# Optimization experiments

Hardware: AMD Instinct MI355X
Metric: run time of the kernel (lower is better)

The kernel has to match this reference:

```python
import jax, jax.numpy as jnp
import numpy as np
from jax import lax

BN_EPS = 1e-5

def _conv(x, w, groups=1, pad=0):
    return lax.conv_general_dilated(
        x, w, window_strides=(1, 1), padding=[(pad, pad), (pad, pad)],
        dimension_numbers=('NCHW', 'OIHW', 'NCHW'), feature_group_count=groups)

def _gather2d(imgf, yi, xi, H, W):
    # imgf: [B,C,H*W] flattened image; yi, xi: [B,C,H,W] int32 corner indices
    valid = (yi >= 0) & (yi < H) & (xi >= 0) & (xi < W)
    yc = jnp.clip(yi, 0, H - 1)
    xc = jnp.clip(xi, 0, W - 1)
    idx = (yc * W + xc).reshape(imgf.shape[0], imgf.shape[1], -1)
    v = jnp.take_along_axis(imgf, idx, axis=2).reshape(yi.shape)
    return jnp.where(valid, v, 0.0)

def _bilinear_sample(img, y, x):
    # img: [B,C,H,W]; y, x: [B,C,H,W] float sample coords (zero outside)
    B, C, H, W = img.shape
    imgf = img.reshape(B, C, H * W)
    y0 = jnp.floor(y)
    x0 = jnp.floor(x)
    wy = y - y0  # weight for y1 corner
    wx = x - x0
    y0i = y0.astype(jnp.int32); y1i = y0i + 1
    x0i = x0.astype(jnp.int32); x1i = x0i + 1
    v00 = _gather2d(imgf, y0i, x0i, H, W)
    v01 = _gather2d(imgf, y0i, x1i, H, W)
    v10 = _gather2d(imgf, y1i, x0i, H, W)
    v11 = _gather2d(imgf, y1i, x1i, H, W)
    return ((1 - wy) * (1 - wx) * v00 + (1 - wy) * wx * v01
            + wy * (1 - wx) * v10 + wy * wx * v11)

def setup_inputs() -> dict:
    key = jax.random.key(0)
    ks = jax.random.split(key, 6)
    B, C, OC, H, W = 4, 64, 64, 256, 256
    return {
        'x': jax.random.normal(ks[0], (B, C, H, W), jnp.float32),
        'dw_weight': jax.random.normal(ks[1], (C, 1, 3, 3), jnp.float32) * 0.2,
        'pw_weight': jax.random.normal(ks[2], (3 * C, C, 1, 1), jnp.float32) * 0.1,
        'weight': jax.random.normal(ks[3], (OC, C, 1, 1), jnp.float32) * 0.1,
        'bias': jax.random.normal(ks[4], (OC,), jnp.float32) * 0.1,
        'gamma': jnp.ones((OC,), jnp.float32),
        'beta': jnp.zeros((OC,), jnp.float32),
    }

def reference(x, dw_weight, pw_weight, weight, bias, gamma, beta):
    B, C, H, W = x.shape
    # DWConv2d: depthwise 3x3 (pad 1) then pointwise 1x1 -> 3C channels
    om = _conv(_conv(x, dw_weight, groups=C, pad=1), pw_weight)
    offset_y = om[:, :C]
    offset_x = om[:, C:2 * C]
    modulator = 2.0 * jax.nn.sigmoid(om[:, 2 * C:])
    max_off = max(H, W) // 4
    offset = jnp.clip(jnp.concatenate([offset_y, offset_x], axis=1), -max_off, max_off)
    # torchvision deform_conv2d layout: [B, og*2, H, W] interleaved (y, x) per offset group
    off = offset.reshape(B, C, 2, H, W)
    hh = jnp.arange(H, dtype=x.dtype)[:, None]
    ww = jnp.arange(W, dtype=x.dtype)[None, :]
    sy = hh + off[:, :, 0]  # [B,C,H,W]
    sx = ww + off[:, :, 1]
    sampled = _bilinear_sample(x, sy, sx) * modulator
    w2 = weight.reshape(weight.shape[0], C)  # 1x1 kernel -> [OC, C]
    out = jnp.einsum('oc,bchw->bohw', w2, sampled) + bias[None, :, None, None]
    # BatchNorm2d (training-mode batch stats) + exact GELU
    mean = out.mean(axis=(0, 2, 3), keepdims=True)
    var = out.var(axis=(0, 2, 3), keepdims=True)
    out = (out - mean) * lax.rsqrt(var + BN_EPS)
    out = out * gamma[None, :, None, None] + beta[None, :, None, None]
    return jax.nn.gelu(out, approximate=False)
```

## Files before the change

kernel.cpp:

```cpp
#include <hip/hip_runtime.h>

#define B_  4
#define C_  64
#define H_  256
#define W_  256
#define HW_ 65536
#define NPIX_ (B_*HW_)
#define NELEM_ (B_*C_*HW_)

#define OMS 200
#define TS  72

typedef __attribute__((ext_vector_type(8))) short short8;
typedef __attribute__((ext_vector_type(4))) float floatx4;

static __device__ __forceinline__ unsigned short f2bf(float f){
  unsigned u = __float_as_uint(f);
  u += 0x7fff + ((u >> 16) & 1);
  return (unsigned short)(u >> 16);
}
static __device__ __forceinline__ float bf2f(unsigned short s){
  return __uint_as_float(((unsigned)s) << 16);
}
static __device__ __forceinline__ unsigned pack2(float a, float b){
  return (unsigned)f2bf(a) | ((unsigned)f2bf(b) << 16);
}

__global__ __launch_bounds__(256) void k_cvtw(
    const float* __restrict__ pw, const float* __restrict__ w2,
    unsigned short* __restrict__ wB)
{
  int i = blockIdx.x*256 + threadIdx.x;
  wB[i] = f2bf(i < 12288 ? pw[i] : w2[i - 12288]);
}

__global__ __launch_bounds__(256) void k_cvtx(
    const float4* __restrict__ X4, uint2* __restrict__ Y)
{
  int i = blockIdx.x*256 + threadIdx.x;
  float4 a = X4[i];
  uint2 u; u.x = pack2(a.x, a.y); u.y = pack2(a.z, a.w);
  Y[i] = u;
}

__global__ __launch_bounds__(256) void k_dwconv(
    const unsigned short* __restrict__ xB,
    const float* __restrict__ dwW,
    unsigned short* __restrict__ t)
{
  int tid = threadIdx.x;
  int bid = ((blockIdx.x & 7) << 9) + (blockIdx.x >> 3);
  int b    = bid >> 10;
  int tile = bid & 1023;
  int h    = tile >> 2;
  int w0   = (tile & 3) << 6;
  int p  = tid & 63;
  int cg = tid >> 6;
  int wg = w0 + p;

  unsigned pk[8];
#pragma unroll
  for (int i = 0; i < 16; ++i){
    int c = cg*16 + i;
    const unsigned short* xp = xB + ((size_t)(b*C_ + c) << 16);
    const float* wp = dwW + c*9;
    float acc = 0.f;
#pragma unroll
    for (int dy = -1; dy <= 1; ++dy){
      int hy = h + dy;
      if ((unsigned)hy >= (unsigned)H_) continue;
      const unsigned short* row = xp + (hy << 8);
#pragma unroll
      for (int dx = -1; dx <= 1; ++dx){
        int wx = wg + dx;
        if ((unsigned)wx >= (unsigned)W_) continue;
        acc += wp[(dy+1)*3 + (dx+1)] * bf2f(row[wx]);
      }
    }
    unsigned short bv = f2bf(acc);
    if (i & 1) pk[i>>1] |= ((unsigned)bv << 16);
    else       pk[i>>1]  = (unsigned)bv;
  }
  size_t rowbase = ((size_t)bid*64 + p)*64 + cg*16;
  uint4 u0; u0.x = pk[0]; u0.y = pk[1]; u0.z = pk[2]; u0.w = pk[3];
  uint4 u1; u1.x = pk[4]; u1.y = pk[5]; u1.z = pk[6]; u1.w = pk[7];
  *(uint4*)(t + rowbase)     = u0;
  *(uint4*)(t + rowbase + 8) = u1;
}

__global__ __launch_bounds__(256, 4) void k_fuse(
    const unsigned short* __restrict__ xB,
    const unsigned short* __restrict__ t,
    const unsigned short* __restrict__ pwB,
    const unsigned short* __restrict__ w2B,
    unsigned short* __restrict__ outB,
    float* __restrict__ gsumS,
    float* __restrict__ gsqS)
{
  __shared__ __align__(16) char lds[27648];
  unsigned short* OM = (unsigned short*)lds;
  unsigned short* T  = (unsigned short*)lds;
  float* red1 = (float*)(lds + 25600);
  float* red2 = (float*)(lds + 25600 + 1024);

  int tid = threadIdx.x;
  int bid = ((blockIdx.x & 7) << 9) + (blockIdx.x >> 3);
  int wv = tid >> 6, lane = tid & 63;
  int mrow = lane & 15, q = lane >> 4;
  int px0 = bid*64;
  int pxw = px0 + wv*16;

  short8 bfrag[2];
#pragma unroll
  for (int kb = 0; kb < 2; ++kb)
    bfrag[kb] = *(const short8*)(t + (size_t)(pxw + mrow)*64 + kb*32 + q*8);

  floatx4 acc[12];
#pragma unroll
  for (int mt = 0; mt < 12; ++mt) acc[mt] = (floatx4){0.f,0.f,0.f,0.f};
#pragma unroll
  for (int kb = 0; kb < 2; ++kb)
#pragma unroll
    for (int mt = 0; mt < 12; ++mt){
      short8 af = *(const short8*)(pwB + (mt*16 + mrow)*64 + kb*32 + q*8);
      acc[mt] = __builtin_amdgcn_mfma_f32_16x16x32_bf16(af, bfrag[kb], acc[mt], 0, 0, 0);
    }

  {
    int omrow = (wv*16 + mrow)*OMS;
#pragma unroll
    for (int mt = 0; mt < 12; ++mt){
      uint2 u; u.x = pack2(acc[mt][0], acc[mt][1]); u.y = pack2(acc[mt][2], acc[mt][3]);
      *(uint2*)(OM + omrow + mt*16 + q*4) = u;
    }
  }
  __syncthreads();

  unsigned pk[8];
  {
    int pl = tid >> 2;
    int cg = tid & 3;
    int px = px0 + pl;
    int b = px >> 16;
    int p = px & (HW_-1);
    int h = p >> 8, w = p & (W_-1);
    int c0 = cg*16;

    const uint4* ob = (const uint4*)(OM + pl*OMS + cg*32);
    uint4 oA = ob[0], oB = ob[1], oC = ob[2], oD = ob[3];
    const uint4* mb = (const uint4*)(OM + pl*OMS + 128 + cg*16);
    uint4 mA = mb[0], mB = mb[1];
    unsigned pr[16] = {oA.x,oA.y,oA.z,oA.w, oB.x,oB.y,oB.z,oB.w,
                       oC.x,oC.y,oC.z,oC.w, oD.x,oD.y,oD.z,oD.w};
    unsigned md[8]  = {mA.x,mA.y,mA.z,mA.w, mB.x,mB.y,mB.z,mB.w};

    const unsigned short* xb = xB + ((size_t)(b*C_) << 16);
    float hf = (float)h, wf = (float)w;
#pragma unroll
    for (int i = 0; i < 16; ++i){
      int c = c0 + i;
      unsigned pair = pr[i];
      float oy = bf2f((unsigned short)(pair & 0xffffu));
      float ox = bf2f((unsigned short)(pair >> 16));
      float mm = bf2f((unsigned short)((md[i>>1] >> ((i&1)*16)) & 0xffffu));
      float mod = 2.f / (1.f + __expf(-mm));
      oy = fminf(fmaxf(oy, -64.f), 64.f);
      ox = fminf(fmaxf(ox, -64.f), 64.f);
      float sy = hf + oy, sx = wf + ox;
      float y0f = floorf(sy), x0f = floorf(sx);
      float wy = sy - y0f, wxr = sx - x0f;
      int y0 = (int)y0f, x0 = (int)x0f;
      bool y0v = ((unsigned)y0     < (unsigned)H_);
      bool y1v = ((unsigned)(y0+1) < (unsigned)H_);
      bool x0v = ((unsigned)x0     < (unsigned)W_);
      bool x1v = ((unsigned)(x0+1) < (unsigned)W_);
      int xc  = min(max(x0, 0), 254);
      bool x0lo = (x0 == xc);
      int yc0 = min(max(y0,   0), 255);
      int yc1 = min(max(y0+1, 0), 255);
      const unsigned short* xp = xb + ((size_t)c << 16);
      unsigned pu0, pu1;
      __builtin_memcpy(&pu0, xp + (yc0 << 8) + xc, 4);
      __builtin_memcpy(&pu1, xp + (yc1 << 8) + xc, 4);
      float lo0 = bf2f((unsigned short)(pu0 & 0xffffu)), hi0 = bf2f((unsigned short)(pu0 >> 16));
      float lo1 = bf2f((unsigned short)(pu1 & 0xffffu)), hi1 = bf2f((unsigned short)(pu1 >> 16));
      float v00 = x0lo ? lo0 : hi0;  v00 = (x0v && y0v) ? v00 : 0.f;
      float v01 = x0lo ? hi0 : lo0;  v01 = (x1v && y0v) ? v01 : 0.f;
      float v10 = x0lo ? lo1 : hi1;  v10 = (x0v && y1v) ? v10 : 0.f;
      float v11 = x0lo ? hi1 : lo1;  v11 = (x1v && y1v) ? v11 : 0.f;
      float sres = (1.f-wy)*((1.f-wxr)*v00 + wxr*v01) + wy*((1.f-wxr)*v10 + wxr*v11);
      unsigned short bv = f2bf(sres * mod);
      if (i & 1) pk[i>>1] |= ((unsigned)bv << 16);
      else       pk[i>>1]  = (unsigned)bv;
    }
  }
  __syncthreads();

  {
    int pl = tid >> 2, cg = tid & 3;
    uint4 u0; u0.x = pk[0]; u0.y = pk[1]; u0.z = pk[2]; u0.w = pk[3];
    uint4 u1; u1.x = pk[4]; u1.y = pk[5]; u1.z = pk[6]; u1.w = pk[7];
    *(uint4*)(T + pl*TS + cg*16)     = u0;
    *(uint4*)(T + pl*TS + cg*16 + 8) = u1;
  }
  __syncthreads();

  short8 a2[2];
#pragma unroll
  for (int kb = 0; kb < 2; ++kb)
    a2[kb] = *(const short8*)(T + (wv*16 + mrow)*TS + kb*32 + q*8);

  floatx4 acc2[4];
#pragma unroll
  for (int nt = 0; nt < 4; ++nt) acc2[nt] = (floatx4){0.f,0.f,0.f,0.f};
#pragma unroll
  for (int kb = 0; kb < 2; ++kb)
#pragma unroll
    for (int nt = 0; nt < 4; ++nt){
      short8 bf = *(const short8*)(w2B + (nt*16 + mrow)*64 + kb*32 + q*8);
      acc2[nt] = __builtin_amdgcn_mfma_f32_16x16x32_bf16(a2[kb], bf, acc2[nt], 0, 0, 0);
    }

  int b   = pxw >> 16;
  int hw0 = pxw & (HW_-1);
#pragma unroll
  for (int nt = 0; nt < 4; ++nt){
    int och = nt*16 + mrow;
    float a0 = acc2[nt][0], a1 = acc2[nt][1], a2v = acc2[nt][2], a3 = acc2[nt][3];
    uint2 u; u.x = pack2(a0, a1); u.y = pack2(a2v, a3);
    *(uint2*)(outB + ((size_t)(b*C_ + och) << 16) + hw0 + q*4) = u;
    float s1 = a0 + a1 + a2v + a3;
    float s2 = a0*a0 + a1*a1 + a2v*a2v + a3*a3;
    s1 += __shfl_xor(s1, 16, 64);  s2 += __shfl_xor(s2, 16, 64);
    s1 += __shfl_xor(s1, 32, 64);  s2 += __shfl_xor(s2, 32, 64);
    if (q == 0){ red1[wv*64 + och] = s1; red2[wv*64 + och] = s2; }
  }
  __syncthreads();
  if (tid < 64){
    float t1 = red1[tid] + red1[64+tid] + red1[128+tid] + red1[192+tid];
    float t2 = red2[tid] + red2[64+tid] + red2[128+tid] + red2[192+tid];
    int slot = blockIdx.x & 31;
    atomicAdd(&gsumS[slot*64 + tid], t1);
    atomicAdd(&gsqS[slot*64 + tid], t2);
  }
}

__global__ void k_finalize(const float* __restrict__ gsumS, const float* __restrict__ gsqS,
                           const float* __restrict__ gamma, const float* __restrict__ beta,
                           float* __restrict__ scale, float* __restrict__ shift)
{
  int o = threadIdx.x;
  if (o < 64){
    float s1 = 0.f, s2 = 0.f;
    for (int s = 0; s < 32; ++s){ s1 += gsumS[s*64 + o]; s2 += gsqS[s*64 + o]; }
    float n = (float)NPIX_;
    float mean = s1 / n;
    float var  = s2 / n - mean*mean;
    float sc = gamma[o] * rsqrtf(var + 1e-5f);
    scale[o] = sc;
    shift[o] = beta[o] - mean*sc;
  }
}

__global__ __launch_bounds__(256) void k_bn_gelu(
    const uint4* __restrict__ outB4,
    const float* __restrict__ scale,
    const float* __restrict__ shift,
    float4* __restrict__ y4)
{
  int i = blockIdx.x*256 + threadIdx.x;
  int och = (i >> 13) & 63;
  float sc = scale[och], sh = shift[och];
  uint4 u = outB4[i];
  float e[8];
  e[0] = bf2f((unsigned short)(u.x & 0xffffu)); e[1] = bf2f((unsigned short)(u.x >> 16));
  e[2] = bf2f((unsigned short)(u.y & 0xffffu)); e[3] = bf2f((unsigned short)(u.y >> 16));
  e[4] = bf2f((unsigned short)(u.z & 0xffffu)); e[5] = bf2f((unsigned short)(u.z >> 16));
  e[6] = bf2f((unsigned short)(u.w & 0xffffu)); e[7] = bf2f((unsigned short)(u.w >> 16));
  float4 o0, o1;
  float a;
  a = e[0]*sc + sh; o0.x = 0.5f*a*(1.f + erff(a*0.70710678118654752f));
  a = e[1]*sc + sh; o0.y = 0.5f*a*(1.f + erff(a*0.70710678118654752f));
  a = e[2]*sc + sh; o0.z = 0.5f*a*(1.f + erff(a*0.70710678118654752f));
  a = e[3]*sc + sh; o0.w = 0.5f*a*(1.f + erff(a*0.70710678118654752f));
  a = e[4]*sc + sh; o1.x = 0.5f*a*(1.f + erff(a*0.70710678118654752f));
  a = e[5]*sc + sh; o1.y = 0.5f*a*(1.f + erff(a*0.70710678118654752f));
  a = e[6]*sc + sh; o1.z = 0.5f*a*(1.f + erff(a*0.70710678118654752f));
  a = e[7]*sc + sh; o1.w = 0.5f*a*(1.f + erff(a*0.70710678118654752f));
  y4[2*i]   = o0;
  y4[2*i+1] = o1;
}

extern "C" void kernel_launch(void* const* d_in, const int* in_sizes, int n_in,
                              void* d_out, int out_size, void* d_ws, size_t ws_size,
                              hipStream_t stream)
{
  (void)in_sizes; (void)n_in; (void)out_size; (void)ws_size;
  const float* x     = (const float*)d_in[0];
  const float* dw    = (const float*)d_in[1];
  const float* pw    = (const float*)d_in[2];
  const float* w2    = (const float*)d_in[3];
  const float* gamma = (const float*)d_in[5];
  const float* beta  = (const float*)d_in[6];

  char* ws = (char*)d_ws;
  unsigned short* xB    = (unsigned short*)ws;
  unsigned short* t     = (unsigned short*)(ws + 33554432);
  unsigned short* outB  = (unsigned short*)(ws + 67108864);
  float*          stats = (float*)(ws + 100663296);
  float* gsumS = stats;
  float* gsqS  = stats + 2048;
  float* scale = stats + 4096;
  float* shift = stats + 4160;
  unsigned short* wB  = (unsigned short*)(ws + 100680192);
  unsigned short* pwB = wB;
  unsigned short* w2B = wB + 12288;

  k_cvtw    <<<64, 256, 0, stream>>>(pw, w2, wB);
  k_cvtx    <<<NELEM_/4/256, 256, 0, stream>>>((const float4*)x, (uint2*)xB);
  hipMemsetAsync(stats, 0, 16384, stream);
  k_dwconv  <<<NPIX_/64, 256, 0, stream>>>(xB, dw, t);
  k_fuse    <<<NPIX_/64, 256, 0, stream>>>(xB, t, pwB, w2B, outB, gsumS, gsqS);
  k_finalize<<<1, 64, 0, stream>>>(gsumS, gsqS, gamma, beta, scale, shift);
  k_bn_gelu <<<NELEM_/8/256, 256, 0, stream>>>((const uint4*)outB, scale, shift,
                                               (float4*)d_out);
}
```

Before: 318.0 us.

## Restructure bilinear gather into batched loads and raise occupancy target

The sampling loop now works in two halves of 8 channels. It computes all addresses and folded bilinear weights first, with the modulator and validity masks merged into the row and column weights, then issues the 16 gathers, then blends. This uses 32-bit byte offsets and shift-based bf16 unpacking. The LDS buffer shrinks by moving the reduction scratch into the reused OM region, and launch bounds ask for 5 blocks per CU instead of 4. The aim is more gathers in flight and higher occupancy, at the risk of register pressure or spills under the tighter launch bound.

After: 320.4 us. About the same (+0.8%).

```diff
diff --git a/kernel.cpp b/kernel.cpp
--- a/kernel.cpp
+++ b/kernel.cpp
@@ -88,7 +88,7 @@
   *(uint4*)(t + rowbase + 8) = u1;
 }
 
-__global__ __launch_bounds__(256, 4) void k_fuse(
+__global__ __launch_bounds__(256, 5) void k_fuse(
     const unsigned short* __restrict__ xB,
     const unsigned short* __restrict__ t,
     const unsigned short* __restrict__ pwB,
@@ -97,11 +97,11 @@
     float* __restrict__ gsumS,
     float* __restrict__ gsqS)
 {
-  __shared__ __align__(16) char lds[27648];
+  __shared__ __align__(16) char lds[25600];
   unsigned short* OM = (unsigned short*)lds;
   unsigned short* T  = (unsigned short*)lds;
-  float* red1 = (float*)(lds + 25600);
-  float* red2 = (float*)(lds + 25600 + 1024);
+  float* red1 = (float*)(lds + 9216);
+  float* red2 = (float*)(lds + 10240);
 
   int tid = threadIdx.x;
   int bid = ((blockIdx.x & 7) << 9) + (blockIdx.x >> 3);
@@ -144,54 +144,69 @@
     int b = px >> 16;
     int p = px & (HW_-1);
     int h = p >> 8, w = p & (W_-1);
-    int c0 = cg*16;
-
-    const uint4* ob = (const uint4*)(OM + pl*OMS + cg*32);
-    uint4 oA = ob[0], oB = ob[1], oC = ob[2], oD = ob[3];
-    const uint4* mb = (const uint4*)(OM + pl*OMS + 128 + cg*16);
-    uint4 mA = mb[0], mB = mb[1];
-    unsigned pr[16] = {oA.x,oA.y,oA.z,oA.w, oB.x,oB.y,oB.z,oB.w,
-                       oC.x,oC.y,oC.z,oC.w, oD.x,oD.y,oD.z,oD.w};
-    unsigned md[8]  = {mA.x,mA.y,mA.z,mA.w, mB.x,mB.y,mB.z,mB.w};
-
-    const unsigned short* xb = xB + ((size_t)(b*C_) << 16);
+
+    const char* xbyte = (const char*)(xB + ((size_t)(b*C_ + cg*16) << 16));
     float hf = (float)h, wf = (float)w;
-#pragma unroll
-    for (int i = 0; i < 16; ++i){
-      int c = c0 + i;
-      unsigned pair = pr[i];
-      float oy = bf2f((unsigned short)(pair & 0xffffu));
-      float ox = bf2f((unsigned short)(pair >> 16));
-      float mm = bf2f((unsigned short)((md[i>>1] >> ((i&1)*16)) & 0xffffu));
-      float mod = 2.f / (1.f + __expf(-mm));
-      oy = fminf(fmaxf(oy, -64.f), 64.f);
-      ox = fminf(fmaxf(ox, -64.f), 64.f);
-      float sy = hf + oy, sx = wf + ox;
-      float y0f = floorf(sy), x0f = floorf(sx);
-      float wy = sy - y0f, wxr = sx - x0f;
-      int y0 = (int)y0f, x0 = (int)x0f;
-      bool y0v = ((unsigned)y0     < (unsigned)H_);
-      bool y1v = ((unsigned)(y0+1) < (unsigned)H_);
-      bool x0v = ((unsigned)x0     < (unsigned)W_);
-      bool x1v = ((unsigned)(x0+1) < (unsigned)W_);
-      int xc  = min(max(x0, 0), 254);
-      bool x0lo = (x0 == xc);
-      int yc0 = min(max(y0,   0), 255);
-      int yc1 = min(max(y0+1, 0), 255);
-      const unsigned short* xp = xb + ((size_t)c << 16);
-      unsigned pu0, pu1;
-      __builtin_memcpy(&pu0, xp + (yc0 << 8) + xc, 4);
-      __builtin_memcpy(&pu1, xp + (yc1 << 8) + xc, 4);
-      float lo0 = bf2f((unsigned short)(pu0 & 0xffffu)), hi0 = bf2f((unsigned short)(pu0 >> 16));
-      float lo1 = bf2f((unsigned short)(pu1 & 0xffffu)), hi1 = bf2f((unsigned short)(pu1 >> 16));
-      float v00 = x0lo ? lo0 : hi0;  v00 = (x0v && y0v) ? v00 : 0.f;
-      float v01 = x0lo ? hi0 : lo0;  v01 = (x1v && y0v) ? v01 : 0.f;
-      float v10 = x0lo ? lo1 : hi1;  v10 = (x0v && y1v) ? v10 : 0.f;
-      float v11 = x0lo ? hi1 : lo1;  v11 = (x1v && y1v) ? v11 : 0.f;
-      float sres = (1.f-wy)*((1.f-wxr)*v00 + wxr*v01) + wy*((1.f-wxr)*v10 + wxr*v11);
-      unsigned short bv = f2bf(sres * mod);
-      if (i & 1) pk[i>>1] |= ((unsigned)bv << 16);
-      else       pk[i>>1]  = (unsigned)bv;
+
+    float rw0[8], rw1[8], cwA[8], cwB[8];
+    unsigned pu0[8], pu1[8];
+
+#pragma unroll
+    for (int half = 0; half < 2; ++half){
+      const uint4* ob = (const uint4*)(OM + pl*OMS + cg*32 + half*16);
+      uint4 oA = ob[0], oB = ob[1];
+      uint4 mv = *(const uint4*)(OM + pl*OMS + 128 + cg*16 + half*8);
+      unsigned pr[8] = {oA.x,oA.y,oA.z,oA.w, oB.x,oB.y,oB.z,oB.w};
+      unsigned md4[4] = {mv.x,mv.y,mv.z,mv.w};
+
+#pragma unroll
+      for (int i = 0; i < 8; ++i){
+        unsigned pair = pr[i];
+        float oy = __uint_as_float(pair << 16);
+        float ox = __uint_as_float(pair & 0xffff0000u);
+        float mm = __uint_as_float((i & 1) ? (md4[i>>1] & 0xffff0000u)
+                                           : (md4[i>>1] << 16));
+        float mod = 2.f / (1.f + __expf(-mm));
+        oy = fminf(fmaxf(oy, -64.f), 64.f);
+        ox = fminf(fmaxf(ox, -64.f), 64.f);
+        float sy = hf + oy, sx = wf + ox;
+        float y0f = floorf(sy), x0f = floorf(sx);
+        float wy = sy - y0f, wxr = sx - x0f;
+        int y0 = (int)y0f, x0 = (int)x0f;
+        int yc0 = min(max(y0,     0), 255);
+        int yc1 = min(max(y0 + 1, 0), 255);
+        int xc  = min(max(x0, 0), 254);
+        bool y0v = ((unsigned)y0       < 256u);
+        bool y1v = ((unsigned)(y0 + 1) < 256u);
+        bool x0v = ((unsigned)x0       < 256u);
+        bool x1v = ((unsigned)(x0 + 1) < 256u);
+        bool x0lo = (x0 == xc);
+        float r0 = y0v ? (1.f - wy) * mod : 0.f;
+        float r1 = y1v ? wy * mod : 0.f;
+        float c0w = x0v ? (1.f - wxr) : 0.f;
+        float c1w = x1v ? wxr : 0.f;
+        rw0[i] = r0; rw1[i] = r1;
+        cwA[i] = x0lo ? c0w : c1w;
+        cwB[i] = x0lo ? c1w : c0w;
+        unsigned cb  = ((unsigned)(half*8 + i)) << 17;
+        unsigned o0  = cb + ((unsigned)yc0 << 9) + ((unsigned)xc << 1);
+        unsigned o1  = cb + ((unsigned)yc1 << 9) + ((unsigned)xc << 1);
+        __builtin_memcpy(&pu0[i], xbyte + o0, 4);
+        __builtin_memcpy(&pu1[i], xbyte + o1, 4);
+      }
+#pragma unroll
+      for (int i = 0; i < 8; ++i){
+        int ci = half*8 + i;
+        float lo0 = __uint_as_float(pu0[i] << 16);
+        float hi0 = __uint_as_float(pu0[i] & 0xffff0000u);
+        float lo1 = __uint_as_float(pu1[i] << 16);
+        float hi1 = __uint_as_float(pu1[i] & 0xffff0000u);
+        float sres = rw0[i] * (cwA[i]*lo0 + cwB[i]*hi0)
+                   + rw1[i] * (cwA[i]*lo1 + cwB[i]*hi1);
+        unsigned short bv = f2bf(sres);
+        if (ci & 1) pk[ci>>1] |= ((unsigned)bv << 16);
+        else        pk[ci>>1]  = (unsigned)bv;
+      }
     }
   }
   __syncthreads();
```
